# Kernel optimization log

Measured on AMD Instinct MI355X. Metric: run time of the kernel, lower is better.

The kernel has to match this reference:

```python
import jax, jax.numpy as jnp
import numpy as np

N = 100000      # nodes
E = 1200000     # edges (every node gets >=1 incoming edge)
DIN = 64
DOUT = 64
EDIM = 16
AVG_D = 2.5649493574615367  # log(avg_in_degree + 1) = log(13)
EPS = 1e-5


def setup_inputs() -> dict:
    key = jax.random.key(0)
    ks = jax.random.split(key, 10)
    h = jax.random.normal(ks[0], (N, DIN), dtype=jnp.float32)
    e = jax.random.normal(ks[1], (E, EDIM), dtype=jnp.float32)
    snorm_n = jax.random.uniform(ks[2], (N, 1), dtype=jnp.float32, minval=0.05, maxval=1.0)
    src = jax.random.randint(ks[3], (E,), 0, N, dtype=jnp.int32)
    # guarantee in-degree >= 1 for every node (DGL reduce requires non-empty mailbox)
    dst = jnp.concatenate([jnp.arange(N, dtype=jnp.int32),
                           jax.random.randint(ks[4], (E - N,), 0, N, dtype=jnp.int32)])
    d_pre_in = 2 * DIN + EDIM  # 144
    d_post_in = (4 * 3 + 1) * DIN  # 832
    W_pre = jax.random.normal(ks[5], (d_pre_in, DIN), dtype=jnp.float32) / np.sqrt(d_pre_in)
    b_pre = jnp.zeros((DIN,), dtype=jnp.float32)
    W_post = jax.random.normal(ks[6], (d_post_in, DOUT), dtype=jnp.float32) / np.sqrt(d_post_in)
    b_post = jnp.zeros((DOUT,), dtype=jnp.float32)
    bn_gamma = jnp.ones((DOUT,), dtype=jnp.float32)
    bn_beta = jnp.zeros((DOUT,), dtype=jnp.float32)
    return {"h": h, "e": e, "snorm_n": snorm_n,
            "W_pre": W_pre, "b_pre": b_pre, "W_post": W_post, "b_post": b_post,
            "bn_gamma": bn_gamma, "bn_beta": bn_beta, "src": src, "dst": dst}


def reference(h, e, snorm_n, W_pre, b_pre, W_post, b_post, bn_gamma, bn_beta, src, dst):
    n = h.shape[0]
    # --- pretrans on edges: MLP(cat[src_feat, dst_feat, edge_feat]) (1 layer, no act) ---
    z = jnp.concatenate([h[src], h[dst], e], axis=1)           # [E, 2*DIN+EDIM]
    m = z @ W_pre + b_pre                                      # [E, DIN] edge messages
    # --- multi-aggregator segment reduce over destination mailboxes ---
    deg = jax.ops.segment_sum(jnp.ones((m.shape[0],), m.dtype), dst, num_segments=n)
    D = deg[:, None]                                           # [N,1], all >= 1
    s1 = jax.ops.segment_sum(m, dst, num_segments=n)
    s2 = jax.ops.segment_sum(m * m, dst, num_segments=n)
    mean = s1 / D
    std = jnp.sqrt(jax.nn.relu(s2 / D - mean * mean) + EPS)
    mx = jax.ops.segment_max(m, dst, num_segments=n)
    mn = jax.ops.segment_min(m, dst, num_segments=n)
    agg = jnp.concatenate([mean, mx, mn, std], axis=1)          # [N, 4*DIN]
    # --- degree scalers: identity, amplification, attenuation ---
    logd = jnp.log(D + 1.0)
    scaled = jnp.concatenate([agg, agg * (logd / AVG_D), agg * (AVG_D / logd)], axis=1)  # [N, 12*DIN]
    # --- posttrans on cat[h, aggregated] (1 layer, no act) ---
    feat = jnp.concatenate([h, scaled], axis=1)                 # [N, 13*DIN]
    out = feat @ W_post + b_post                                # [N, DOUT]
    out = out * snorm_n                                        # graph norm
    # BatchNorm1d in training mode (batch stats over nodes, biased var)
    mu = out.mean(axis=0)
    var = out.var(axis=0)
    out = (out - mu) / jnp.sqrt(var + 1e-5) * bn_gamma + bn_beta
    # dropout p=0.0 -> identity
    return out
```

## Files before the change

### kernel.cpp

```cpp
#include <hip/hip_runtime.h>
#include <hip/hip_bf16.h>
#include <math.h>

#define N_NODES 100000
#define N_EDGES 1200000
#define NT_EDGE 75000
#define NPASS   3
#define TILES_PER_PASS 25000
#define ROWS_PER_PASS  400000
#define NT_POST 6250
#define AVG_D   2.5649493574615367f
#define EPSV    1e-5f

typedef __attribute__((ext_vector_type(8))) short short8;
typedef __attribute__((ext_vector_type(4))) float f32x4;

#define OFF_DEG       0u
#define OFF_ROWLOCAL  400000u
#define OFF_BSUM      800000u
#define OFF_BOFFS     802048u
#define OFF_ROWSTART  804096u
#define OFF_CURSOR    1204096u
#define OFF_EIDS      1604096u
#define OFF_AB        6404096u
#define OFF_BNACC     7204096u
#define OFF_BNFIN     7204608u
#define OFF_HB        7205120u
#define OFF_MBUF      20005120u
#define OFF_AGG       71205120u
#define OFF_CARRY     OFF_BSUM
#define OFF_OUTPRE    OFF_MBUF

__device__ __forceinline__ short f2b(float f){
    union { float f; unsigned u; } c; c.f = f;
    unsigned u = c.u;
    unsigned r = (u + 0x7fffu + ((u >> 16) & 1u)) >> 16;
    return (short)r;
}
__device__ __forceinline__ float b2f(unsigned u16){
    union { unsigned u; float f; } c; c.u = u16 << 16;
    return c.f;
}
__device__ __forceinline__ unsigned pk(float a, float b){
    return ((unsigned)(unsigned short)f2b(a)) | (((unsigned)(unsigned short)f2b(b)) << 16);
}

__global__ void k_prep(const int* __restrict__ dst, unsigned* __restrict__ deg,
                       const float* __restrict__ h, unsigned short* __restrict__ hb){
    int i = blockIdx.x*256 + threadIdx.x;
    if (i < N_EDGES) atomicAdd(&deg[dst[i]], 1u);
    if (i < 800000){
        const float4* p = (const float4*)h + (size_t)i*2;
        float4 u0 = p[0], u1 = p[1];
        uint4 o;
        o.x = pk(u0.x,u0.y); o.y = pk(u0.z,u0.w);
        o.z = pk(u1.x,u1.y); o.w = pk(u1.z,u1.w);
        ((uint4*)hb)[i] = o;
    }
}
__global__ void k_scan1(const unsigned* __restrict__ deg, unsigned* __restrict__ rowlocal,
                        unsigned* __restrict__ bsum){
    __shared__ unsigned s[256];
    int t = threadIdx.x; int i = blockIdx.x*256 + t;
    unsigned d = (i < N_NODES) ? deg[i] : 0u;
    s[t] = d; __syncthreads();
    for (int off=1; off<256; off<<=1){
        unsigned v = (t>=off) ? s[t-off] : 0u; __syncthreads();
        s[t] += v; __syncthreads();
    }
    if (i < N_NODES) rowlocal[i] = s[t] - d;
    if (t == 255) bsum[blockIdx.x] = s[255];
}
__global__ void k_scan2(const unsigned* __restrict__ bsum, unsigned* __restrict__ boffs){
    __shared__ unsigned s[512];
    int t = threadIdx.x;
    unsigned v = (t < 391) ? bsum[t] : 0u;
    s[t] = v; __syncthreads();
    for (int off=1; off<512; off<<=1){
        unsigned x = (t>=off) ? s[t-off] : 0u; __syncthreads();
        s[t] += x; __syncthreads();
    }
    boffs[t] = s[t] - v;
}
__global__ void k_scan3(const unsigned* __restrict__ rowlocal, const unsigned* __restrict__ boffs,
                        unsigned* __restrict__ rowstart){
    int i = blockIdx.x*256 + threadIdx.x;
    if (i < N_NODES) rowstart[i] = rowlocal[i] + boffs[i>>8];
}
__global__ void k_scatter(const int* __restrict__ dst, const unsigned* __restrict__ rowstart,
                          unsigned* __restrict__ cursor, unsigned* __restrict__ eids){
    int i = blockIdx.x*256 + threadIdx.x;
    if (i < N_EDGES){
        int d = dst[i];
        unsigned pos = rowstart[d] + atomicAdd(&cursor[d], 1u);
        eids[pos] = (unsigned)i;
    }
}

__global__ __launch_bounds__(256) void k_edge(
    const unsigned short* __restrict__ hb, const float* __restrict__ e_in,
    const float* __restrict__ W_pre, const float* __restrict__ b_pre,
    const unsigned* __restrict__ eids, const int* __restrict__ src,
    const int* __restrict__ dst, unsigned short* __restrict__ mbuf, int pass)
{
    int tid = threadIdx.x;
    int wv = tid>>6, l = tid&63;
    int lr = l&15, lg = l>>4;

    short8 B[5][4];
    #pragma unroll
    for (int ks=0; ks<5; ks++){
        #pragma unroll
        for (int cg=0; cg<4; cg++){
            short8 b;
            #pragma unroll
            for (int e=0; e<8; e++){
                int k = ks*32 + lg*8 + e;
                b[e] = (k < 144) ? f2b(W_pre[k*64 + cg*16 + lr]) : (short)0;
            }
            B[ks][cg] = b;
        }
    }
    float bias[4];
    #pragma unroll
    for (int cg=0; cg<4; cg++) bias[cg] = b_pre[cg*16 + lr];

    int t0 = pass*TILES_PER_PASS;
    int gw = blockIdx.x*4 + wv;
    int nw = gridDim.x*4;
    for (int t = gw; t < TILES_PER_PASS; t += nw){
        int gt = t0 + t;
        unsigned eid = eids[gt*16 + lr];
        int sn = src[eid], dn = dst[eid];
        const unsigned short* ps = hb + (size_t)sn*64 + lg*8;
        const unsigned short* pd = hb + (size_t)dn*64 + lg*8;
        f32x4 acc[4];
        #pragma unroll
        for (int cg=0; cg<4; cg++) acc[cg] = (f32x4){0.f,0.f,0.f,0.f};

        short8 A;
        A = *(const short8*)ps;
        #pragma unroll
        for (int cg=0; cg<4; cg++) acc[cg] = __builtin_amdgcn_mfma_f32_16x16x32_bf16(A, B[0][cg], acc[cg], 0,0,0);
        A = *(const short8*)(ps + 32);
        #pragma unroll
        for (int cg=0; cg<4; cg++) acc[cg] = __builtin_amdgcn_mfma_f32_16x16x32_bf16(A, B[1][cg], acc[cg], 0,0,0);
        A = *(const short8*)pd;
        #pragma unroll
        for (int cg=0; cg<4; cg++) acc[cg] = __builtin_amdgcn_mfma_f32_16x16x32_bf16(A, B[2][cg], acc[cg], 0,0,0);
        A = *(const short8*)(pd + 32);
        #pragma unroll
        for (int cg=0; cg<4; cg++) acc[cg] = __builtin_amdgcn_mfma_f32_16x16x32_bf16(A, B[3][cg], acc[cg], 0,0,0);
        {
            short8 A4 = {0,0,0,0,0,0,0,0};
            if (lg < 2){
                const float* pe = e_in + (size_t)eid*16 + lg*8;
                float4 u0 = *(const float4*)pe, u1 = *(const float4*)(pe+4);
                A4[0]=f2b(u0.x); A4[1]=f2b(u0.y); A4[2]=f2b(u0.z); A4[3]=f2b(u0.w);
                A4[4]=f2b(u1.x); A4[5]=f2b(u1.y); A4[6]=f2b(u1.z); A4[7]=f2b(u1.w);
            }
            #pragma unroll
            for (int cg=0; cg<4; cg++) acc[cg] = __builtin_amdgcn_mfma_f32_16x16x32_bf16(A4, B[4][cg], acc[cg], 0,0,0);
        }
        #pragma unroll
        for (int r=0; r<4; r++){
            size_t row = (size_t)t*16 + lg*4 + r;
            #pragma unroll
            for (int cg=0; cg<4; cg++)
                mbuf[row*64 + cg*16 + lr] = (unsigned short)f2b(acc[cg][r] + bias[cg]);
        }
    }
}

__global__ __launch_bounds__(256) void k_agg(
    const unsigned short* __restrict__ mbuf, const unsigned* __restrict__ rowstart,
    const unsigned* __restrict__ deg, unsigned short* __restrict__ agg,
    float* __restrict__ ab, float* __restrict__ carry, int pass)
{
    int wv = threadIdx.x>>6, l = threadIdx.x&63;
    int node = blockIdx.x*4 + wv;
    int hf = l>>5, c = l&31;
    unsigned start = rowstart[node];
    int d = (int)deg[node];
    unsigned end = start + (unsigned)d;
    unsigned lo = (unsigned)pass * ROWS_PER_PASS;
    unsigned hi = lo + ROWS_PER_PASS;
    if (end <= lo || start >= hi) return;
    unsigned a = start < lo ? lo : start;
    unsigned b = end > hi ? hi : end;
    int n = (int)(b - a);
    const unsigned short* p = mbuf + (size_t)(a - lo)*64 + 2*c;
    float s1a=0.f,s2a=0.f,mxa=-3.402823466e38f,mna=3.402823466e38f;
    float s1b=0.f,s2b=0.f,mxb=-3.402823466e38f,mnb=3.402823466e38f;
    for (int i=hf; i<n; i+=2){
        unsigned v = *(const unsigned*)(p + (size_t)i*64);
        float va = b2f(v & 0xffffu), vb = b2f(v >> 16);
        s1a += va; s2a = fmaf(va,va,s2a); mxa = fmaxf(mxa,va); mna = fminf(mna,va);
        s1b += vb; s2b = fmaf(vb,vb,s2b); mxb = fmaxf(mxb,vb); mnb = fminf(mnb,vb);
    }
    s1a += __shfl_xor(s1a,32); s2a += __shfl_xor(s2a,32);
    mxa = fmaxf(mxa,__shfl_xor(mxa,32)); mna = fminf(mna,__shfl_xor(mna,32));
    s1b += __shfl_xor(s1b,32); s2b += __shfl_xor(s2b,32);
    mxb = fmaxf(mxb,__shfl_xor(mxb,32)); mnb = fminf(mnb,__shfl_xor(mnb,32));
    if (l < 32){
        if (start < lo){
            const float* cb = carry + (size_t)(pass-1)*256;
            s1a += cb[      2*c];   s1b += cb[      2*c+1];
            s2a += cb[ 64 + 2*c];   s2b += cb[ 64 + 2*c+1];
            mxa = fmaxf(mxa, cb[128 + 2*c]); mxb = fmaxf(mxb, cb[128 + 2*c+1]);
            mna = fminf(mna, cb[192 + 2*c]); mnb = fminf(mnb, cb[192 + 2*c+1]);
        }
        if (end > hi){
            float* cb = carry + (size_t)pass*256;
            cb[      2*c] = s1a;  cb[      2*c+1] = s1b;
            cb[ 64 + 2*c] = s2a;  cb[ 64 + 2*c+1] = s2b;
            cb[128 + 2*c] = mxa;  cb[128 + 2*c+1] = mxb;
            cb[192 + 2*c] = mna;  cb[192 + 2*c+1] = mnb;
        } else {
            float D = (float)d;
            float meana = s1a/D, meanb = s1b/D;
            float sda = sqrtf(fmaxf(s2a/D - meana*meana, 0.f) + EPSV);
            float sdb = sqrtf(fmaxf(s2b/D - meanb*meanb, 0.f) + EPSV);
            unsigned* ag = (unsigned*)(agg + (size_t)node*256) + c;
            ag[ 0] = pk(meana, meanb);
            ag[32] = pk(mxa,  mxb);
            ag[64] = pk(mna,  mnb);
            ag[96] = pk(sda,  sdb);
            if (c == 0){
                float logd = logf(D + 1.f);
                ab[node*2]   = logd / AVG_D;
                ab[node*2+1] = AVG_D / logd;
            }
        }
    }
}

__global__ __launch_bounds__(256) void k_post(
    const unsigned short* __restrict__ hb, const unsigned short* __restrict__ agg,
    const float* __restrict__ ab, const float* __restrict__ snorm,
    const float* __restrict__ W_post, const float* __restrict__ b_post,
    float* __restrict__ out_pre, float* __restrict__ bn_acc)
{
    int tid = threadIdx.x;
    int cg = tid>>6;
    int l = tid&63, lr = l&15, lg = l>>4;
    int col = cg*16 + lr;

    short8 Bm[10], B2[8], B3[8];
    #pragma unroll
    for (int ks=0; ks<10; ks++){
        short8 b;
        #pragma unroll
        for (int e=0; e<8; e++){
            int row = ks*32 + lg*8 + e;
            b[e] = f2b(W_post[row*64 + col]);
        }
        Bm[ks] = b;
    }
    #pragma unroll
    for (int ks=0; ks<8; ks++){
        short8 b, c;
        #pragma unroll
        for (int e=0; e<8; e++){
            int row = ks*32 + lg*8 + e;
            b[e] = f2b(W_post[(320+row)*64 + col]);
            c[e] = f2b(W_post[(576+row)*64 + col]);
        }
        B2[ks] = b; B3[ks] = c;
    }
    float bias = b_post[col];
    float bs = 0.f, bq = 0.f;

    for (int t = blockIdx.x; t < NT_POST; t += gridDim.x){
        int nodeA = t*16 + lr;
        f32x4 aM = {0.f,0.f,0.f,0.f}, a2 = {0.f,0.f,0.f,0.f}, a3 = {0.f,0.f,0.f,0.f};
        #pragma unroll
        for (int ks=0; ks<2; ks++){
            short8 A = *(const short8*)(hb + (size_t)nodeA*64 + ks*32 + lg*8);
            aM = __builtin_amdgcn_mfma_f32_16x16x32_bf16(A, Bm[ks], aM, 0,0,0);
        }
        #pragma unroll
        for (int ks=0; ks<8; ks++){
            short8 A = *(const short8*)(agg + (size_t)nodeA*256 + ks*32 + lg*8);
            aM = __builtin_amdgcn_mfma_f32_16x16x32_bf16(A, Bm[2+ks], aM, 0,0,0);
            a2 = __builtin_amdgcn_mfma_f32_16x16x32_bf16(A, B2[ks],  a2, 0,0,0);
            a3 = __builtin_amdgcn_mfma_f32_16x16x32_bf16(A, B3[ks],  a3, 0,0,0);
        }
        #pragma unroll
        for (int r=0; r<4; r++){
            int node = t*16 + lg*4 + r;
            float av = ab[node*2], bv = ab[node*2+1];
            float v = (aM[r] + av*a2[r] + bv*a3[r] + bias) * snorm[node];
            out_pre[(size_t)node*64 + col] = v;
            bs += v; bq = fmaf(v,v,bq);
        }
    }
    bs += __shfl_xor(bs, 16); bs += __shfl_xor(bs, 32);
    bq += __shfl_xor(bq, 16); bq += __shfl_xor(bq, 32);
    if (l < 16){
        atomicAdd(&bn_acc[cg*16 + l], bs);
        atomicAdd(&bn_acc[64 + cg*16 + l], bq);
    }
}

__global__ void k_bnfin(const float* __restrict__ bn_acc, const float* __restrict__ gamma,
                        const float* __restrict__ beta, float* __restrict__ bn_fin){
    int c = threadIdx.x;
    float invN = 1.f/(float)N_NODES;
    float mu = bn_acc[c]*invN;
    float ms = bn_acc[64+c]*invN;
    float var = fmaxf(ms - mu*mu, 0.f);
    float scale = gamma[c] / sqrtf(var + 1e-5f);
    bn_fin[c] = scale;
    bn_fin[64+c] = beta[c] - mu*scale;
}
__global__ void k_apply(const float* __restrict__ out_pre, const float* __restrict__ bn_fin,
                        float* __restrict__ out){
    int i = blockIdx.x*256 + threadIdx.x;
    int c4 = (i & 15) * 4;
    float4 v  = ((const float4*)out_pre)[i];
    float4 sc = *(const float4*)&bn_fin[c4];
    float4 sh = *(const float4*)&bn_fin[64 + c4];
    float4 o;
    o.x = fmaf(v.x, sc.x, sh.x); o.y = fmaf(v.y, sc.y, sh.y);
    o.z = fmaf(v.z, sc.z, sh.z); o.w = fmaf(v.w, sc.w, sh.w);
    ((float4*)out)[i] = o;
}

extern "C" void kernel_launch(void* const* d_in, const int* in_sizes, int n_in,
                              void* d_out, int out_size, void* d_ws, size_t ws_size,
                              hipStream_t stream)
{
    const float* h      = (const float*)d_in[0];
    const float* e_in   = (const float*)d_in[1];
    const float* snorm  = (const float*)d_in[2];
    const float* W_pre  = (const float*)d_in[3];
    const float* b_pre  = (const float*)d_in[4];
    const float* W_post = (const float*)d_in[5];
    const float* b_post = (const float*)d_in[6];
    const float* gamma  = (const float*)d_in[7];
    const float* beta   = (const float*)d_in[8];
    const int*   src    = (const int*)d_in[9];
    const int*   dst    = (const int*)d_in[10];

    char* ws = (char*)d_ws;
    unsigned* deg      = (unsigned*)(ws + OFF_DEG);
    unsigned* rowlocal = (unsigned*)(ws + OFF_ROWLOCAL);
    unsigned* bsum     = (unsigned*)(ws + OFF_BSUM);
    unsigned* boffs    = (unsigned*)(ws + OFF_BOFFS);
    unsigned* rowstart = (unsigned*)(ws + OFF_ROWSTART);
    unsigned* cursor   = (unsigned*)(ws + OFF_CURSOR);
    unsigned* eids     = (unsigned*)(ws + OFF_EIDS);
    float*    abuf     = (float*)(ws + OFF_AB);
    float*    bnacc    = (float*)(ws + OFF_BNACC);
    float*    bnfin    = (float*)(ws + OFF_BNFIN);
    unsigned short* hb   = (unsigned short*)(ws + OFF_HB);
    unsigned short* mbuf = (unsigned short*)(ws + OFF_MBUF);
    unsigned short* aggp = (unsigned short*)(ws + OFF_AGG);
    float*    carry    = (float*)(ws + OFF_CARRY);
    float*    outpre   = (float*)(ws + OFF_OUTPRE);

    hipMemsetAsync(ws + OFF_DEG,    0, 400000, stream);
    hipMemsetAsync(ws + OFF_CURSOR, 0, 400000, stream);
    hipMemsetAsync(ws + OFF_BNACC,  0, 512,    stream);

    k_prep   <<<4688, 256, 0, stream>>>(dst, deg, h, hb);
    k_scan1  <<<391,  256, 0, stream>>>(deg, rowlocal, bsum);
    k_scan2  <<<1,    512, 0, stream>>>(bsum, boffs);
    k_scan3  <<<391,  256, 0, stream>>>(rowlocal, boffs, rowstart);
    k_scatter<<<4688, 256, 0, stream>>>(dst, rowstart, cursor, eids);

    for (int pass = 0; pass < NPASS; pass++){
        k_edge <<<1024, 256, 0, stream>>>(hb, e_in, W_pre, b_pre, eids, src, dst, mbuf, pass);
        k_agg  <<<25000,256, 0, stream>>>(mbuf, rowstart, deg, aggp, abuf, carry, pass);
    }

    k_post   <<<512,  256, 0, stream>>>(hb, aggp, abuf, snorm, W_post, b_post, outpre, bnacc);
    k_bnfin  <<<1,    64,  0, stream>>>(bnacc, gamma, beta, bnfin);
    k_apply  <<<6250, 256, 0, stream>>>(outpre, bnfin, (float*)d_out);
}
```

Measured before the change: 593.1 us.

## Pack edge id, src and dst into sorted records; one tile per wave

The scatter kernel now writes a record holding edge id, source and destination in destination-sorted order. The edge kernel reads that record directly instead of chasing two dependent gathers through src/dst. The edge kernel also drops its grid-stride loop and launches one 16-edge tile per wave, and k_post gets twice as many blocks. This trades a larger scatter write and re-loading W_pre per tile for shorter dependent-load chains and more parallelism.

```diff
diff --git a/kernel.cpp b/kernel.cpp
--- a/kernel.cpp
+++ b/kernel.cpp
@@ -15,19 +15,21 @@
 typedef __attribute__((ext_vector_type(8))) short short8;
 typedef __attribute__((ext_vector_type(4))) float f32x4;
 
+struct ERec { unsigned eid, sn, dn; };
+
 #define OFF_DEG       0u
 #define OFF_ROWLOCAL  400000u
 #define OFF_BSUM      800000u
 #define OFF_BOFFS     802048u
 #define OFF_ROWSTART  804096u
 #define OFF_CURSOR    1204096u
-#define OFF_EIDS      1604096u
-#define OFF_AB        6404096u
-#define OFF_BNACC     7204096u
-#define OFF_BNFIN     7204608u
-#define OFF_HB        7205120u
-#define OFF_MBUF      20005120u
-#define OFF_AGG       71205120u
+#define OFF_EREC      1604096u
+#define OFF_AB        16004096u
+#define OFF_BNACC     16804096u
+#define OFF_BNFIN     16804608u
+#define OFF_HB        16805120u
+#define OFF_MBUF      29605120u
+#define OFF_AGG       80805120u
 #define OFF_CARRY     OFF_BSUM
 #define OFF_OUTPRE    OFF_MBUF
 
@@ -87,21 +89,23 @@
     int i = blockIdx.x*256 + threadIdx.x;
     if (i < N_NODES) rowstart[i] = rowlocal[i] + boffs[i>>8];
 }
-__global__ void k_scatter(const int* __restrict__ dst, const unsigned* __restrict__ rowstart,
-                          unsigned* __restrict__ cursor, unsigned* __restrict__ eids){
+__global__ void k_scatter(const int* __restrict__ src, const int* __restrict__ dst,
+                          const unsigned* __restrict__ rowstart,
+                          unsigned* __restrict__ cursor, ERec* __restrict__ erec){
     int i = blockIdx.x*256 + threadIdx.x;
     if (i < N_EDGES){
         int d = dst[i];
+        int s = src[i];
         unsigned pos = rowstart[d] + atomicAdd(&cursor[d], 1u);
-        eids[pos] = (unsigned)i;
+        ERec r; r.eid = (unsigned)i; r.sn = (unsigned)s; r.dn = (unsigned)d;
+        erec[pos] = r;
     }
 }
 
 __global__ __launch_bounds__(256) void k_edge(
     const unsigned short* __restrict__ hb, const float* __restrict__ e_in,
     const float* __restrict__ W_pre, const float* __restrict__ b_pre,
-    const unsigned* __restrict__ eids, const int* __restrict__ src,
-    const int* __restrict__ dst, unsigned short* __restrict__ mbuf, int pass)
+    const ERec* __restrict__ erec, unsigned short* __restrict__ mbuf, int pass)
 {
     int tid = threadIdx.x;
     int wv = tid>>6, l = tid&63;
@@ -125,50 +129,47 @@
     #pragma unroll
     for (int cg=0; cg<4; cg++) bias[cg] = b_pre[cg*16 + lr];
 
-    int t0 = pass*TILES_PER_PASS;
-    int gw = blockIdx.x*4 + wv;
-    int nw = gridDim.x*4;
-    for (int t = gw; t < TILES_PER_PASS; t += nw){
-        int gt = t0 + t;
-        unsigned eid = eids[gt*16 + lr];
-        int sn = src[eid], dn = dst[eid];
-        const unsigned short* ps = hb + (size_t)sn*64 + lg*8;
-        const unsigned short* pd = hb + (size_t)dn*64 + lg*8;
-        f32x4 acc[4];
-        #pragma unroll
-        for (int cg=0; cg<4; cg++) acc[cg] = (f32x4){0.f,0.f,0.f,0.f};
-
-        short8 A;
-        A = *(const short8*)ps;
-        #pragma unroll
-        for (int cg=0; cg<4; cg++) acc[cg] = __builtin_amdgcn_mfma_f32_16x16x32_bf16(A, B[0][cg], acc[cg], 0,0,0);
-        A = *(const short8*)(ps + 32);
-        #pragma unroll
-        for (int cg=0; cg<4; cg++) acc[cg] = __builtin_amdgcn_mfma_f32_16x16x32_bf16(A, B[1][cg], acc[cg], 0,0,0);
-        A = *(const short8*)pd;
-        #pragma unroll
-        for (int cg=0; cg<4; cg++) acc[cg] = __builtin_amdgcn_mfma_f32_16x16x32_bf16(A, B[2][cg], acc[cg], 0,0,0);
-        A = *(const short8*)(pd + 32);
-        #pragma unroll
-        for (int cg=0; cg<4; cg++) acc[cg] = __builtin_amdgcn_mfma_f32_16x16x32_bf16(A, B[3][cg], acc[cg], 0,0,0);
-        {
-            short8 A4 = {0,0,0,0,0,0,0,0};
-            if (lg < 2){
-                const float* pe = e_in + (size_t)eid*16 + lg*8;
-                float4 u0 = *(const float4*)pe, u1 = *(const float4*)(pe+4);
-                A4[0]=f2b(u0.x); A4[1]=f2b(u0.y); A4[2]=f2b(u0.z); A4[3]=f2b(u0.w);
-                A4[4]=f2b(u1.x); A4[5]=f2b(u1.y); A4[6]=f2b(u1.z); A4[7]=f2b(u1.w);
-            }
-            #pragma unroll
-            for (int cg=0; cg<4; cg++) acc[cg] = __builtin_amdgcn_mfma_f32_16x16x32_bf16(A4, B[4][cg], acc[cg], 0,0,0);
-        }
-        #pragma unroll
-        for (int r=0; r<4; r++){
-            size_t row = (size_t)t*16 + lg*4 + r;
-            #pragma unroll
-            for (int cg=0; cg<4; cg++)
-                mbuf[row*64 + cg*16 + lr] = (unsigned short)f2b(acc[cg][r] + bias[cg]);
-        }
+    int t = blockIdx.x*4 + wv;
+    if (t >= TILES_PER_PASS) return;
+    int gt = pass*TILES_PER_PASS + t;
+
+    ERec r = erec[gt*16 + lr];
+    const unsigned short* ps = hb + (size_t)r.sn*64 + lg*8;
+    const unsigned short* pd = hb + (size_t)r.dn*64 + lg*8;
+    f32x4 acc[4];
+    #pragma unroll
+    for (int cg=0; cg<4; cg++) acc[cg] = (f32x4){0.f,0.f,0.f,0.f};
+
+    short8 A;
+    A = *(const short8*)ps;
+    #pragma unroll
+    for (int cg=0; cg<4; cg++) acc[cg] = __builtin_amdgcn_mfma_f32_16x16x32_bf16(A, B[0][cg], acc[cg], 0,0,0);
+    A = *(const short8*)(ps + 32);
+    #pragma unroll
+    for (int cg=0; cg<4; cg++) acc[cg] = __builtin_amdgcn_mfma_f32_16x16x32_bf16(A, B[1][cg], acc[cg], 0,0,0);
+    A = *(const short8*)pd;
+    #pragma unroll
+    for (int cg=0; cg<4; cg++) acc[cg] = __builtin_amdgcn_mfma_f32_16x16x32_bf16(A, B[2][cg], acc[cg], 0,0,0);
+    A = *(const short8*)(pd + 32);
+    #pragma unroll
+    for (int cg=0; cg<4; cg++) acc[cg] = __builtin_amdgcn_mfma_f32_16x16x32_bf16(A, B[3][cg], acc[cg], 0,0,0);
+    {
+        short8 A4 = {0,0,0,0,0,0,0,0};
+        if (lg < 2){
+            const float* pe = e_in + (size_t)r.eid*16 + lg*8;
+            float4 u0 = *(const float4*)pe, u1 = *(const float4*)(pe+4);
+            A4[0]=f2b(u0.x); A4[1]=f2b(u0.y); A4[2]=f2b(u0.z); A4[3]=f2b(u0.w);
+            A4[4]=f2b(u1.x); A4[5]=f2b(u1.y); A4[6]=f2b(u1.z); A4[7]=f2b(u1.w);
+        }
+        #pragma unroll
+        for (int cg=0; cg<4; cg++) acc[cg] = __builtin_amdgcn_mfma_f32_16x16x32_bf16(A4, B[4][cg], acc[cg], 0,0,0);
+    }
+    #pragma unroll
+    for (int rr=0; rr<4; rr++){
+        size_t row = (size_t)t*16 + lg*4 + rr;
+        #pragma unroll
+        for (int cg=0; cg<4; cg++)
+            mbuf[row*64 + cg*16 + lr] = (unsigned short)f2b(acc[cg][rr] + bias[cg]);
     }
 }
 
@@ -350,7 +351,7 @@
     unsigned* boffs    = (unsigned*)(ws + OFF_BOFFS);
     unsigned* rowstart = (unsigned*)(ws + OFF_ROWSTART);
     unsigned* cursor   = (unsigned*)(ws + OFF_CURSOR);
-    unsigned* eids     = (unsigned*)(ws + OFF_EIDS);
+    ERec*     erec     = (ERec*)(ws + OFF_EREC);
     float*    abuf     = (float*)(ws + OFF_AB);
     float*    bnacc    = (float*)(ws + OFF_BNACC);
     float*    bnfin    = (float*)(ws + OFF_BNFIN);
@@ -368,14 +369,14 @@
     k_scan1  <<<391,  256, 0, stream>>>(deg, rowlocal, bsum);
     k_scan2  <<<1,    512, 0, stream>>>(bsum, boffs);
     k_scan3  <<<391,  256, 0, stream>>>(rowlocal, boffs, rowstart);
-    k_scatter<<<4688, 256, 0, stream>>>(dst, rowstart, cursor, eids);
+    k_scatter<<<4688, 256, 0, stream>>>(src, dst, rowstart, cursor, erec);
 
     for (int pass = 0; pass < NPASS; pass++){
-        k_edge <<<1024, 256, 0, stream>>>(hb, e_in, W_pre, b_pre, eids, src, dst, mbuf, pass);
+        k_edge <<<6250, 256, 0, stream>>>(hb, e_in, W_pre, b_pre, erec, mbuf, pass);
         k_agg  <<<25000,256, 0, stream>>>(mbuf, rowstart, deg, aggp, abuf, carry, pass);
     }
 
-    k_post   <<<512,  256, 0, stream>>>(hb, aggp, abuf, snorm, W_post, b_post, outpre, bnacc);
+    k_post   <<<1024, 256, 0, stream>>>(hb, aggp, abuf, snorm, W_post, b_post, outpre, bnacc);
     k_bnfin  <<<1,    64,  0, stream>>>(bnacc, gamma, beta, bnfin);
     k_apply  <<<6250, 256, 0, stream>>>(outpre, bnfin, (float*)d_out);
 }
```

New measurement: 731.4 us. 23.3% more time.
